# Performance work log

Measured on AMD Instinct MI355X. Metric: run time of the kernel, lower is better.

The kernel has to match this reference:

```python
import jax, jax.numpy as jnp
import numpy as np

jax.config.update("jax_enable_x64", True)  # loss accumulates int64 squared index diffs (~1e14)

PATCH, STRIDE = 7, 1


def extract_patches(img, p, s):
    # img: [b, c, h, w] -> patches [b, N, c*p*p], N = oh*ow (normalize_patch='none')
    pat = jax.lax.conv_general_dilated_patches(img, (p, p), (s, s), 'VALID')  # [b, c*p*p, oh, ow]
    b, d = pat.shape[0], pat.shape[1]
    return pat.reshape(b, d, -1).transpose(0, 2, 1)


def bisect_left(a, v):
    # Exact replica of np.searchsorted(a, v, side='left') binary search,
    # applied (as in the original code) to an UNSORTED int array `a`.
    # a: [N] int, v: [M] int -> [M] insertion indices in [0, N].
    N = a.shape[0]
    lo = jnp.zeros(v.shape, jnp.int64)
    hi = jnp.full(v.shape, N, jnp.int64)
    n_iter = int(np.ceil(np.log2(N))) + 1
    for _ in range(n_iter):
        mid = (lo + hi) // 2
        am = a[jnp.clip(mid, 0, N - 1)]
        go = lo < hi
        pred = am < v
        lo = jnp.where(go & pred, mid + 1, lo)
        hi = jnp.where(go & (~pred), mid, hi)
    return lo


def nearest_vals(a, v):
    # Vectorized find_nearest(a, v_i) for all v_i. a: [N], v: [M].
    N = a.shape[0]
    idx = bisect_left(a, v)
    a_prev = a[jnp.clip(idx - 1, 0, N - 1)]
    a_at = a[jnp.clip(idx, 0, N - 1)]
    take_prev = (idx > 0) & ((idx == N) | (jnp.abs(v - a_prev) < jnp.abs(v - a_at)))
    return jnp.where(take_prev, a_prev, a_at)


def reference(x, y, rand):
    # rand: [b, d, num_proj]; per-batch projection matrix, normalized by unbiased column std
    rand = rand / jnp.std(rand, axis=1, keepdims=True, ddof=1)
    xp = extract_patches(x, PATCH, STRIDE)  # [b, N, d]
    yp = extract_patches(y, PATCH, STRIDE)  # [b, N, d]
    proj_x = jnp.einsum('bnd,bdp->bnp', xp, rand)
    proj_y = jnp.einsum('bnd,bdp->bnp', yp, rand)
    # Original overwrites projections with argsort indices; only j=0 is used
    # because of the early return inside the projection loop.
    ai = jnp.argsort(proj_x[:, :, 0], axis=1).astype(jnp.int64)  # [b, N]
    at = jnp.argsort(proj_y[:, :, 0], axis=1).astype(jnp.int64)  # [b, N]
    nearest = jax.vmap(nearest_vals)(at, ai)  # [b, N]
    N = ai.shape[1]
    per_image = jnp.sum((ai - nearest) ** 2, axis=1) / N  # int sum -> float
    return jnp.mean(per_image)  # batch_reduction='mean'


def setup_inputs() -> dict:
    key = jax.random.key(0)
    k1, k2, k3 = jax.random.split(key, 3)
    b, c, h, w = 4, 3, 256, 256
    d = c * PATCH * PATCH  # 147
    x = jax.random.normal(k1, (b, c, h, w), dtype=jnp.float32)
    y = jax.random.normal(k2, (b, c, h, w), dtype=jnp.float32)
    rand = jax.random.normal(k3, (b, d, 1), dtype=jnp.float32)
    return {"x": x, "y": y, "rand": rand}
```

## Files before the change

### kernel.cpp

```cpp
#include <hip/hip_runtime.h>
#include <stdint.h>

#define OH 250
#define OW 250
#define NPTS (OH*OW)
#define NSEG 4
#define D 147
#define CH 3
#define IMH 256
#define IMW 256
#define NITER 17
#define NBUCK 4096
#define SIG0 12.124355652982141

typedef unsigned long long u64;
typedef unsigned int u32;

#define OFF_REC   0UL
#define OFF_SREC  2000000UL
#define OFF_A     4000000UL
#define OFF_HIST  5000000UL
#define OFF_BASES 5065536UL
#define OFF_CURS  5131088UL
#define OFF_WTS   5196624UL
#define OFF_SUMS  5201328UL
#define WS_NEED   5201360UL

__device__ __forceinline__ u64 packd(double f) {
  u64 u = (u64)__double_as_longlong(f);
  return (u & 0x8000000000000000ULL) ? ~u : (u | 0x8000000000000000ULL);
}

__device__ __forceinline__ int bucket_of(u64 rec) {
  u64 t = rec & ~0x1FFFFULL;
  u64 bits = (t & 0x8000000000000000ULL) ? (t & 0x7FFFFFFFFFFFFFFFULL) : ~t;
  double v = __longlong_as_double((long long)bits);
  double z = (v + 4.0 * SIG0) * ((double)NBUCK / (8.0 * SIG0));
  int b = (z <= 0.0) ? 0 : (int)z;
  if (b > NBUCK - 1) b = NBUCK - 1;
  return b;
}

__global__ __launch_bounds__(256) void prep_kern(const float* __restrict__ rnd,
                                                 double* __restrict__ wts,
                                                 u32* __restrict__ hist,
                                                 u64* __restrict__ sums) {
  int t = threadIdx.x;
  if (blockIdx.x < 4) {
    __shared__ double red[256];
    int b = blockIdx.x;
    double val = (t < D) ? (double)rnd[b * D + t] : 0.0;
    red[t] = val;
    __syncthreads();
    for (int s = 128; s > 0; s >>= 1) { if (t < s) red[t] += red[t + s]; __syncthreads(); }
    double mean = red[0] / (double)D;
    __syncthreads();
    double dv = (t < D) ? (val - mean) : 0.0;
    red[t] = dv * dv;
    __syncthreads();
    for (int s = 128; s > 0; s >>= 1) { if (t < s) red[t] += red[t + s]; __syncthreads(); }
    double stdv = sqrt(red[0] / (double)(D - 1));
    if (t < D) wts[b * D + t] = val / stdv;
  } else {
    int g = (blockIdx.x - 4) * 256 + t;
    if (g < NSEG * NBUCK) hist[g] = 0u;
    if (g < 4) sums[g] = 0ULL;
  }
}

__global__ __launch_bounds__(256) void conv_kern(const float* __restrict__ y,
                                                 const double* __restrict__ wts,
                                                 u64* __restrict__ recs,
                                                 u32* __restrict__ hist) {
  __shared__ float tile[CH][22][22];
  __shared__ double w[D];
  __shared__ u32 lh[NBUCK];
  int b = blockIdx.z;
  const float* in = y + (size_t)b * CH * IMH * IMW;
  int bi = blockIdx.y * 16, bj = blockIdx.x * 16;
  int tid = threadIdx.y * 16 + threadIdx.x;
  for (int k = tid; k < NBUCK; k += 256) lh[k] = 0u;
  if (tid < D) w[tid] = wts[b * D + tid];
  for (int c = 0; c < CH; ++c)
    for (int t = tid; t < 22 * 22; t += 256) {
      int rr = t / 22, cc = t - rr * 22;
      int r = bi + rr, col = bj + cc;
      float v = 0.f;
      if (r < IMH && col < IMW) v = in[((size_t)c * IMH + r) * IMW + col];
      tile[c][rr][cc] = v;
    }
  __syncthreads();
  int i = bi + threadIdx.y, j = bj + threadIdx.x;
  if (i < OH && j < OW) {
    double acc = 0.0;
    #pragma unroll
    for (int c = 0; c < CH; ++c)
      #pragma unroll
      for (int ph = 0; ph < 7; ++ph)
        #pragma unroll
        for (int pw = 0; pw < 7; ++pw)
          acc = fma((double)tile[c][threadIdx.y + ph][threadIdx.x + pw],
                    w[c * 49 + ph * 7 + pw], acc);
    int n = i * OW + j;
    u64 rec = (packd(acc) & ~0x1FFFFULL) | (u64)(u32)n;
    recs[(size_t)b * NPTS + n] = rec;
    atomicAdd(&lh[bucket_of(rec)], 1u);
  }
  __syncthreads();
  for (int k = tid; k < NBUCK; k += 256) {
    u32 c = lh[k];
    if (c) atomicAdd(&hist[b * NBUCK + k], c);
  }
}

__global__ __launch_bounds__(1024) void scan_kern(const u32* __restrict__ hist,
                                                  u32* __restrict__ bases,
                                                  u32* __restrict__ curs) {
  __shared__ u32 part[1024];
  int seg = blockIdx.x, t = threadIdx.x;
  u32 c[4];
  #pragma unroll
  for (int m = 0; m < 4; ++m) c[m] = hist[seg * NBUCK + 4 * t + m];
  u32 s = c[0] + c[1] + c[2] + c[3];
  part[t] = s;
  __syncthreads();
  for (int off = 1; off < 1024; off <<= 1) {
    u32 v = (t >= off) ? part[t - off] : 0u;
    __syncthreads();
    part[t] += v;
    __syncthreads();
  }
  u32 ex = part[t] - s;
  #pragma unroll
  for (int m = 0; m < 4; ++m) {
    bases[seg * (NBUCK + 1) + 4 * t + m] = ex;
    curs[seg * NBUCK + 4 * t + m] = ex;
    ex += c[m];
  }
  if (t == 1023) bases[seg * (NBUCK + 1) + NBUCK] = ex;
}

__global__ __launch_bounds__(256) void scatter_kern(const u64* __restrict__ recs,
                                                    u32* __restrict__ curs,
                                                    u64* __restrict__ srec) {
  int seg = blockIdx.y;
  int e = blockIdx.x * 256 + threadIdx.x;
  if (e < NPTS) {
    u64 rec = recs[(size_t)seg * NPTS + e];
    int bk = bucket_of(rec);
    u32 pos = atomicAdd(&curs[seg * NBUCK + bk], 1u);
    srec[(size_t)seg * NPTS + pos] = rec;
  }
}

__global__ __launch_bounds__(512) void bsort_kern(const u64* __restrict__ srec,
                                                  const u32* __restrict__ bases,
                                                  u32* __restrict__ a) {
  __shared__ u64 buf[8][512];
  int wid = threadIdx.x >> 6, lane = threadIdx.x & 63;
  int w = blockIdx.x * 8 + wid;
  int seg = w >> 12, bk = w & (NBUCK - 1);
  u32 b0 = bases[seg * (NBUCK + 1) + bk];
  u32 b1 = bases[seg * (NBUCK + 1) + bk + 1];
  int n = (int)(b1 - b0);
  const u64* src = srec + (size_t)seg * NPTS + b0;
  u32* dst = a + (size_t)seg * NPTS + b0;
  bool uselds = (n <= 512);
  if (uselds) for (int i = lane; i < n; i += 64) buf[wid][i] = src[i];
  __syncthreads();
  if (uselds) {
    for (int i = lane; i < n; i += 64) {
      u64 x = buf[wid][i];
      int r = 0;
      for (int j = 0; j < n; ++j) r += (buf[wid][j] < x);
      dst[r] = (u32)(x & 0x1FFFFULL);
    }
  } else {
    for (int i = lane; i < n; i += 64) {
      u64 x = src[i];
      int r = 0;
      for (int j = 0; j < n; ++j) r += (src[j] < x);
      dst[r] = (u32)(x & 0x1FFFFULL);
    }
  }
}

__global__ __launch_bounds__(256) void loss_kern(const u32* __restrict__ a_all,
                                                 u64* __restrict__ sums) {
  int b = blockIdx.y;
  int v = blockIdx.x * 256 + threadIdx.x;
  const u32* a = a_all + (size_t)b * NPTS;
  long long term = 0;
  if (v < NPTS) {
    int lo = 0, hi = NPTS;
    #pragma unroll
    for (int it = 0; it < NITER; ++it) {
      int mid = (lo + hi) >> 1;
      int cm = mid > NPTS - 1 ? NPTS - 1 : mid;
      int am = (int)a[cm];
      bool go = lo < hi;
      if (go) {
        if (am < v) lo = mid + 1;
        else        hi = mid;
      }
    }
    int pi = lo - 1; if (pi < 0) pi = 0; if (pi > NPTS - 1) pi = NPTS - 1;
    int ci = lo;     if (ci > NPTS - 1) ci = NPTS - 1;
    int ap = (int)a[pi], aa = (int)a[ci];
    int d1 = v - ap; if (d1 < 0) d1 = -d1;
    int d2 = v - aa; if (d2 < 0) d2 = -d2;
    bool take_prev = (lo > 0) && ((lo == NPTS) || (d1 < d2));
    int nearest = take_prev ? ap : aa;
    long long d = (long long)(v - nearest);
    term = d * d;
  }
  for (int off = 32; off > 0; off >>= 1) term += __shfl_down(term, off, 64);
  __shared__ long long part[4];
  int lane = threadIdx.x & 63, wid = threadIdx.x >> 6;
  if (lane == 0) part[wid] = term;
  __syncthreads();
  if (threadIdx.x == 0) {
    long long tot = part[0] + part[1] + part[2] + part[3];
    atomicAdd(&sums[b], (u64)tot);
  }
}

__global__ void final_kern(const u64* __restrict__ sums, float* __restrict__ out) {
  if (threadIdx.x == 0 && blockIdx.x == 0) {
    double l = 0.0;
    for (int b = 0; b < 4; ++b) l += (double)(long long)sums[b] / (double)NPTS;
    out[0] = (float)(l / 4.0);
  }
}

__global__ void guard_kern(float* __restrict__ out) {
  if (threadIdx.x == 0 && blockIdx.x == 0) out[0] = 9.0e12f;
}

extern "C" void kernel_launch(void* const* d_in, const int* in_sizes, int n_in,
                              void* d_out, int out_size, void* d_ws, size_t ws_size,
                              hipStream_t stream) {
  (void)in_sizes; (void)n_in; (void)out_size;
  if (ws_size < WS_NEED) { guard_kern<<<1, 64, 0, stream>>>((float*)d_out); return; }
  const float* y   = (const float*)d_in[1];
  const float* rnd = (const float*)d_in[2];

  char* ws = (char*)d_ws;
  u64* recs   = (u64*)(ws + OFF_REC);
  u64* srec   = (u64*)(ws + OFF_SREC);
  u32* a      = (u32*)(ws + OFF_A);
  u32* hist   = (u32*)(ws + OFF_HIST);
  u32* bases  = (u32*)(ws + OFF_BASES);
  u32* curs   = (u32*)(ws + OFF_CURS);
  double* wts = (double*)(ws + OFF_WTS);
  u64* sums   = (u64*)(ws + OFF_SUMS);

  prep_kern<<<68, 256, 0, stream>>>(rnd, wts, hist, sums);
  conv_kern<<<dim3(16, 16, NSEG), dim3(16, 16), 0, stream>>>(y, wts, recs, hist);
  scan_kern<<<NSEG, 1024, 0, stream>>>(hist, bases, curs);
  scatter_kern<<<dim3((NPTS + 255) / 256, NSEG), 256, 0, stream>>>(recs, curs, srec);
  bsort_kern<<<NSEG * NBUCK / 8, 512, 0, stream>>>(srec, bases, a);
  loss_kern<<<dim3((NPTS + 255) / 256, NSEG), 256, 0, stream>>>(a, sums);
  final_kern<<<1, 64, 0, stream>>>(sums, (float*)d_out);
}
```

Measured before the change: 137.6 us.

## Fuse all pipeline stages into one cooperative kernel with grid syncs

Replaces the seven separate launches (prep, conv, scan, scatter, bucket sort, loss, final) with a single cooperative kernel of 256 blocks of 512 threads that separates the phases with grid-wide syncs. Weight normalisation is done per block with wave shuffles, the histogram uses block-local shared atomics, and the final reduction happens in-kernel. The aim is to remove launch gaps and per-kernel tail effects. In exchange, each phase is limited to fixed grid parallelism, grid.sync adds its own cost, and a fallback keeps the old multi-kernel path if the cooperative launch fails.

```diff
diff --git a/kernel.cpp b/kernel.cpp
--- a/kernel.cpp
+++ b/kernel.cpp
@@ -1,5 +1,8 @@
 #include <hip/hip_runtime.h>
+#include <hip/hip_cooperative_groups.h>
 #include <stdint.h>
+
+namespace cg = cooperative_groups;
 
 #define OH 250
 #define OW 250
@@ -12,6 +15,8 @@
 #define NITER 17
 #define NBUCK 4096
 #define SIG0 12.124355652982141
+#define GRD 256
+#define BLK 512
 
 typedef unsigned long long u64;
 typedef unsigned int u32;
@@ -39,6 +44,217 @@
   int b = (z <= 0.0) ? 0 : (int)z;
   if (b > NBUCK - 1) b = NBUCK - 1;
   return b;
+}
+
+__global__ __launch_bounds__(BLK, 2) void fused_kern(
+    const float* __restrict__ y, const float* __restrict__ rnd,
+    u64* __restrict__ recs, u64* __restrict__ srec, u32* __restrict__ aidx,
+    u32* __restrict__ hist, u32* __restrict__ bases, u32* __restrict__ curs,
+    u64* __restrict__ sums, float* __restrict__ out) {
+  cg::grid_group grid = cg::this_grid();
+  __shared__ double w[NSEG][D];
+  __shared__ __align__(16) char sh[32768];
+  float (*tile)[22][38] = (float (*)[22][38])sh;
+  u32* lhist = (u32*)(sh + 10048);
+  u64 (*bbuf)[512] = (u64 (*)[512])sh;
+  u32* spart = (u32*)sh;
+  __shared__ long long lsums[NSEG];
+
+  int tid = threadIdx.x, bid = blockIdx.x;
+  int lane = tid & 63, wid = tid >> 6;
+
+  if (wid < NSEG) {
+    int s = wid;
+    double v0 = (double)rnd[s * D + lane];
+    double v1 = (lane + 64 < D) ? (double)rnd[s * D + lane + 64] : 0.0;
+    double v2 = (lane + 128 < D) ? (double)rnd[s * D + lane + 128] : 0.0;
+    double sm = v0 + v1 + v2;
+    for (int o = 32; o > 0; o >>= 1) sm += __shfl_down(sm, o, 64);
+    sm = __shfl(sm, 0, 64);
+    double mean = sm / (double)D;
+    double d0 = v0 - mean;
+    double d1 = (lane + 64 < D) ? v1 - mean : 0.0;
+    double d2 = (lane + 128 < D) ? v2 - mean : 0.0;
+    double ss = d0 * d0 + d1 * d1 + d2 * d2;
+    for (int o = 32; o > 0; o >>= 1) ss += __shfl_down(ss, o, 64);
+    ss = __shfl(ss, 0, 64);
+    double stdv = sqrt(ss / (double)(D - 1));
+    w[s][lane] = v0 / stdv;
+    if (lane + 64 < D) w[s][lane + 64] = v1 / stdv;
+    if (lane + 128 < D) w[s][lane + 128] = v2 / stdv;
+  }
+  {
+    int g = bid * BLK + tid;
+    if (g < NSEG * NBUCK) hist[g] = 0u;
+    if (g < NSEG) sums[g] = 0ULL;
+  }
+  grid.sync();
+
+  for (int k = tid; k < NBUCK; k += BLK) lhist[k] = 0u;
+  int T0 = 2 * bid;
+  int seg = T0 >> 7;
+  const float* in = y + (size_t)seg * CH * IMH * IMW;
+  __syncthreads();
+  for (int r = 0; r < 2; ++r) {
+    int tsub = (T0 + r) & 127;
+    int bi = (tsub >> 3) * 16, bj = (tsub & 7) * 32;
+    for (int t = tid; t < CH * 22 * 38; t += BLK) {
+      int c = t / (22 * 38), rem = t % (22 * 38);
+      int rr = rem / 38, cc = rem % 38;
+      int rI = bi + rr, cI = bj + cc;
+      float v = 0.f;
+      if (rI < IMH && cI < IMW) v = in[((size_t)c * IMH + rI) * IMW + cI];
+      tile[c][rr][cc] = v;
+    }
+    __syncthreads();
+    int ty = tid >> 5, tx = tid & 31;
+    int i = bi + ty, j = bj + tx;
+    if (i < OH && j < OW) {
+      double acc = 0.0;
+      #pragma unroll
+      for (int c = 0; c < CH; ++c)
+        #pragma unroll
+        for (int ph = 0; ph < 7; ++ph)
+          #pragma unroll
+          for (int pw = 0; pw < 7; ++pw)
+            acc = fma((double)tile[c][ty + ph][tx + pw], w[seg][c * 49 + ph * 7 + pw], acc);
+      int n = i * OW + j;
+      u64 rec = (packd(acc) & ~0x1FFFFULL) | (u64)(u32)n;
+      recs[(size_t)seg * NPTS + n] = rec;
+      atomicAdd(&lhist[bucket_of(rec)], 1u);
+    }
+    __syncthreads();
+  }
+  for (int k = tid; k < NBUCK; k += BLK) {
+    u32 c = lhist[k];
+    if (c) atomicAdd(&hist[seg * NBUCK + k], c);
+  }
+  grid.sync();
+
+  if (bid < NSEG) {
+    int s = bid;
+    u32 c[8]; u32 run = 0;
+    #pragma unroll
+    for (int m = 0; m < 8; ++m) { c[m] = hist[s * NBUCK + 8 * tid + m]; run += c[m]; }
+    spart[tid] = run;
+    __syncthreads();
+    for (int off = 1; off < BLK; off <<= 1) {
+      u32 v = (tid >= off) ? spart[tid - off] : 0u;
+      __syncthreads();
+      spart[tid] += v;
+      __syncthreads();
+    }
+    u32 ex = spart[tid] - run;
+    #pragma unroll
+    for (int m = 0; m < 8; ++m) {
+      bases[s * (NBUCK + 1) + 8 * tid + m] = ex;
+      curs[s * NBUCK + 8 * tid + m] = ex;
+      ex += c[m];
+    }
+    if (tid == BLK - 1) bases[s * (NBUCK + 1) + NBUCK] = ex;
+  }
+  grid.sync();
+
+  {
+    int g = bid * BLK + tid;
+    #pragma unroll
+    for (int rep = 0; rep < 2; ++rep) {
+      int e = g + rep * (GRD * BLK);
+      if (e < NSEG * NPTS) {
+        u64 rec = recs[e];
+        int s = e / NPTS;
+        int bk = bucket_of(rec);
+        u32 pos = atomicAdd(&curs[s * NBUCK + bk], 1u);
+        srec[(size_t)s * NPTS + pos] = rec;
+      }
+    }
+  }
+  grid.sync();
+
+  {
+    int gw = bid * 8 + wid;
+    for (int q = 0; q < 8; ++q) {
+      int B = gw + q * 2048;
+      int s = B >> 12, bk = B & (NBUCK - 1);
+      u32 b0 = bases[s * (NBUCK + 1) + bk];
+      u32 b1 = bases[s * (NBUCK + 1) + bk + 1];
+      int n = (int)(b1 - b0);
+      const u64* src = srec + (size_t)s * NPTS + b0;
+      u32* dst = aidx + (size_t)s * NPTS + b0;
+      __syncthreads();
+      if (n <= 512) for (int i = lane; i < n; i += 64) bbuf[wid][i] = src[i];
+      __syncthreads();
+      if (n <= 512) {
+        for (int i = lane; i < n; i += 64) {
+          u64 x = bbuf[wid][i]; int rk = 0;
+          for (int jj = 0; jj < n; ++jj) rk += (bbuf[wid][jj] < x);
+          dst[rk] = (u32)(x & 0x1FFFFULL);
+        }
+      } else {
+        for (int i = lane; i < n; i += 64) {
+          u64 x = src[i]; int rk = 0;
+          for (int jj = 0; jj < n; ++jj) rk += (src[jj] < x);
+          dst[rk] = (u32)(x & 0x1FFFFULL);
+        }
+      }
+    }
+  }
+  grid.sync();
+
+  if (tid < NSEG) lsums[tid] = 0;
+  __syncthreads();
+  {
+    int g = bid * BLK + tid;
+    int v1g = g + GRD * BLK;
+    bool a1 = v1g < NSEG * NPTS;
+    int s0 = g / NPTS, s1 = a1 ? v1g / NPTS : 0;
+    int vv0 = g - s0 * NPTS, vv1 = v1g - s1 * NPTS;
+    const u32* A0 = aidx + (size_t)s0 * NPTS;
+    const u32* A1 = aidx + (size_t)s1 * NPTS;
+    int lo0 = 0, hi0 = NPTS, lo1 = 0, hi1 = NPTS;
+    #pragma unroll
+    for (int it = 0; it < NITER; ++it) {
+      int mid0 = (lo0 + hi0) >> 1, mid1 = (lo1 + hi1) >> 1;
+      int cm0 = mid0 > NPTS - 1 ? NPTS - 1 : mid0;
+      int cm1 = mid1 > NPTS - 1 ? NPTS - 1 : mid1;
+      int am0 = (int)A0[cm0];
+      int am1 = (int)A1[cm1];
+      if (lo0 < hi0) { if (am0 < vv0) lo0 = mid0 + 1; else hi0 = mid0; }
+      if (lo1 < hi1) { if (am1 < vv1) lo1 = mid1 + 1; else hi1 = mid1; }
+    }
+    long long t0, t1;
+    {
+      int pi = lo0 - 1; if (pi < 0) pi = 0; if (pi > NPTS - 1) pi = NPTS - 1;
+      int ci = lo0;     if (ci > NPTS - 1) ci = NPTS - 1;
+      int ap = (int)A0[pi], aa = (int)A0[ci];
+      int d1 = vv0 - ap; if (d1 < 0) d1 = -d1;
+      int d2 = vv0 - aa; if (d2 < 0) d2 = -d2;
+      bool tp = (lo0 > 0) && ((lo0 == NPTS) || (d1 < d2));
+      long long dd = (long long)(vv0 - (tp ? ap : aa));
+      t0 = dd * dd;
+    }
+    {
+      int pi = lo1 - 1; if (pi < 0) pi = 0; if (pi > NPTS - 1) pi = NPTS - 1;
+      int ci = lo1;     if (ci > NPTS - 1) ci = NPTS - 1;
+      int ap = (int)A1[pi], aa = (int)A1[ci];
+      int d1 = vv1 - ap; if (d1 < 0) d1 = -d1;
+      int d2 = vv1 - aa; if (d2 < 0) d2 = -d2;
+      bool tp = (lo1 > 0) && ((lo1 == NPTS) || (d1 < d2));
+      long long dd = (long long)(vv1 - (tp ? ap : aa));
+      t1 = dd * dd;
+    }
+    atomicAdd((u64*)&lsums[s0], (u64)t0);
+    if (a1) atomicAdd((u64*)&lsums[s1], (u64)t1);
+  }
+  __syncthreads();
+  if (tid < NSEG && lsums[tid]) atomicAdd(&sums[tid], (u64)lsums[tid]);
+  grid.sync();
+
+  if (bid == 0 && tid == 0) {
+    double l = 0.0;
+    for (int b = 0; b < NSEG; ++b) l += (double)(long long)sums[b] / (double)NPTS;
+    out[0] = (float)(l / 4.0);
+  }
 }
 
 __global__ __launch_bounds__(256) void prep_kern(const float* __restrict__ rnd,
@@ -248,18 +464,25 @@
   char* ws = (char*)d_ws;
   u64* recs   = (u64*)(ws + OFF_REC);
   u64* srec   = (u64*)(ws + OFF_SREC);
-  u32* a      = (u32*)(ws + OFF_A);
+  u32* aidx   = (u32*)(ws + OFF_A);
   u32* hist   = (u32*)(ws + OFF_HIST);
   u32* bases  = (u32*)(ws + OFF_BASES);
   u32* curs   = (u32*)(ws + OFF_CURS);
   double* wts = (double*)(ws + OFF_WTS);
   u64* sums   = (u64*)(ws + OFF_SUMS);
+  float* out  = (float*)d_out;
+
+  void* args[] = { (void*)&y, (void*)&rnd, (void*)&recs, (void*)&srec, (void*)&aidx,
+                   (void*)&hist, (void*)&bases, (void*)&curs, (void*)&sums, (void*)&out };
+  hipError_t err = hipLaunchCooperativeKernel((const void*)fused_kern,
+                                              dim3(GRD), dim3(BLK), args, 0, stream);
+  if (err == hipSuccess) return;
 
   prep_kern<<<68, 256, 0, stream>>>(rnd, wts, hist, sums);
   conv_kern<<<dim3(16, 16, NSEG), dim3(16, 16), 0, stream>>>(y, wts, recs, hist);
   scan_kern<<<NSEG, 1024, 0, stream>>>(hist, bases, curs);
   scatter_kern<<<dim3((NPTS + 255) / 256, NSEG), 256, 0, stream>>>(recs, curs, srec);
-  bsort_kern<<<NSEG * NBUCK / 8, 512, 0, stream>>>(srec, bases, a);
-  loss_kern<<<dim3((NPTS + 255) / 256, NSEG), 256, 0, stream>>>(a, sums);
-  final_kern<<<1, 64, 0, stream>>>(sums, (float*)d_out);
-}
+  bsort_kern<<<NSEG * NBUCK / 8, 512, 0, stream>>>(srec, bases, aidx);
+  loss_kern<<<dim3((NPTS + 255) / 256, NSEG), 256, 0, stream>>>(aidx, sums);
+  final_kern<<<1, 64, 0, stream>>>(sums, out);
+}
```

Result: slower. 284.9 us (+107.1%).

## Fuse prep, scan and final kernels via last-block tickets and memset

Applied to the files above, without the earlier changes.

Drops the separate prep, scan and final launches. Each conv block now normalizes the projection weights itself with wave shuffles. The last conv block, picked by an atomic ticket, runs the histogram prefix scan. The last loss block computes the final mean. Control buffers are zeroed with one hipMemsetAsync, and scatter now adds the bucket base to a zero-started cursor. This cuts launch count and inter-kernel gaps, at the cost of redundant weight normalization per block and a serial single-block scan tail.

```diff
diff --git a/kernel.cpp b/kernel.cpp
--- a/kernel.cpp
+++ b/kernel.cpp
@@ -19,12 +19,14 @@
 #define OFF_REC   0UL
 #define OFF_SREC  2000000UL
 #define OFF_A     4000000UL
+#define OFF_CTRL  5000000UL
 #define OFF_HIST  5000000UL
 #define OFF_BASES 5065536UL
 #define OFF_CURS  5131088UL
-#define OFF_WTS   5196624UL
-#define OFF_SUMS  5201328UL
-#define WS_NEED   5201360UL
+#define OFF_SUMS  5196624UL
+#define OFF_TICK  5196656UL
+#define CTRL_LEN  196664UL
+#define WS_NEED   5196664UL
 
 __device__ __forceinline__ u64 packd(double f) {
   u64 u = (u64)__double_as_longlong(f);
@@ -41,46 +43,42 @@
   return b;
 }
 
-__global__ __launch_bounds__(256) void prep_kern(const float* __restrict__ rnd,
-                                                 double* __restrict__ wts,
+__global__ __launch_bounds__(256) void conv_kern(const float* __restrict__ y,
+                                                 const float* __restrict__ rnd,
+                                                 u64* __restrict__ recs,
                                                  u32* __restrict__ hist,
-                                                 u64* __restrict__ sums) {
-  int t = threadIdx.x;
-  if (blockIdx.x < 4) {
-    __shared__ double red[256];
-    int b = blockIdx.x;
-    double val = (t < D) ? (double)rnd[b * D + t] : 0.0;
-    red[t] = val;
-    __syncthreads();
-    for (int s = 128; s > 0; s >>= 1) { if (t < s) red[t] += red[t + s]; __syncthreads(); }
-    double mean = red[0] / (double)D;
-    __syncthreads();
-    double dv = (t < D) ? (val - mean) : 0.0;
-    red[t] = dv * dv;
-    __syncthreads();
-    for (int s = 128; s > 0; s >>= 1) { if (t < s) red[t] += red[t + s]; __syncthreads(); }
-    double stdv = sqrt(red[0] / (double)(D - 1));
-    if (t < D) wts[b * D + t] = val / stdv;
-  } else {
-    int g = (blockIdx.x - 4) * 256 + t;
-    if (g < NSEG * NBUCK) hist[g] = 0u;
-    if (g < 4) sums[g] = 0ULL;
-  }
-}
-
-__global__ __launch_bounds__(256) void conv_kern(const float* __restrict__ y,
-                                                 const double* __restrict__ wts,
-                                                 u64* __restrict__ recs,
-                                                 u32* __restrict__ hist) {
+                                                 u32* __restrict__ bases,
+                                                 u32* __restrict__ tick) {
   __shared__ float tile[CH][22][22];
   __shared__ double w[D];
   __shared__ u32 lh[NBUCK];
+  __shared__ u32 spart[256];
+  __shared__ u32 rank_s;
   int b = blockIdx.z;
   const float* in = y + (size_t)b * CH * IMH * IMW;
   int bi = blockIdx.y * 16, bj = blockIdx.x * 16;
   int tid = threadIdx.y * 16 + threadIdx.x;
+  int lane = tid & 63;
+
+  {
+    double v0 = (double)rnd[b * D + lane];
+    double v1 = (double)rnd[b * D + lane + 64];
+    double v2 = (lane + 128 < D) ? (double)rnd[b * D + lane + 128] : 0.0;
+    double sm = v0 + v1 + v2;
+    #pragma unroll
+    for (int o = 32; o > 0; o >>= 1) sm += __shfl_xor(sm, o, 64);
+    double mean = sm / (double)D;
+    double d0 = v0 - mean, d1 = v1 - mean;
+    double d2 = (lane + 128 < D) ? (v2 - mean) : 0.0;
+    double ss = d0 * d0 + d1 * d1 + d2 * d2;
+    #pragma unroll
+    for (int o = 32; o > 0; o >>= 1) ss += __shfl_xor(ss, o, 64);
+    double stdv = sqrt(ss / (double)(D - 1));
+    w[lane] = v0 / stdv;
+    w[lane + 64] = v1 / stdv;
+    if (lane + 128 < D) w[lane + 128] = v2 / stdv;
+  }
   for (int k = tid; k < NBUCK; k += 256) lh[k] = 0u;
-  if (tid < D) w[tid] = wts[b * D + tid];
   for (int c = 0; c < CH; ++c)
     for (int t = tid; t < 22 * 22; t += 256) {
       int rr = t / 22, cc = t - rr * 22;
@@ -111,36 +109,40 @@
     u32 c = lh[k];
     if (c) atomicAdd(&hist[b * NBUCK + k], c);
   }
-}
-
-__global__ __launch_bounds__(1024) void scan_kern(const u32* __restrict__ hist,
-                                                  u32* __restrict__ bases,
-                                                  u32* __restrict__ curs) {
-  __shared__ u32 part[1024];
-  int seg = blockIdx.x, t = threadIdx.x;
-  u32 c[4];
-  #pragma unroll
-  for (int m = 0; m < 4; ++m) c[m] = hist[seg * NBUCK + 4 * t + m];
-  u32 s = c[0] + c[1] + c[2] + c[3];
-  part[t] = s;
-  __syncthreads();
-  for (int off = 1; off < 1024; off <<= 1) {
-    u32 v = (t >= off) ? part[t - off] : 0u;
+  __threadfence();
+  if (tid == 0) rank_s = atomicAdd(&tick[0], 1u);
+  __syncthreads();
+  if (rank_s != 16 * 16 * NSEG - 1) return;
+  __threadfence();
+  for (int s2 = 0; s2 < NSEG; ++s2) {
+    u32 c[16]; u32 run = 0;
+    #pragma unroll
+    for (int m = 0; m < 16; ++m) {
+      c[m] = __hip_atomic_load(&hist[s2 * NBUCK + 16 * tid + m],
+                               __ATOMIC_RELAXED, __HIP_MEMORY_SCOPE_AGENT);
+      run += c[m];
+    }
+    spart[tid] = run;
     __syncthreads();
-    part[t] += v;
+    for (int off = 1; off < 256; off <<= 1) {
+      u32 v = (tid >= off) ? spart[tid - off] : 0u;
+      __syncthreads();
+      spart[tid] += v;
+      __syncthreads();
+    }
+    u32 ex = spart[tid] - run;
+    #pragma unroll
+    for (int m = 0; m < 16; ++m) {
+      bases[s2 * (NBUCK + 1) + 16 * tid + m] = ex;
+      ex += c[m];
+    }
+    if (tid == 255) bases[s2 * (NBUCK + 1) + NBUCK] = ex;
     __syncthreads();
   }
-  u32 ex = part[t] - s;
-  #pragma unroll
-  for (int m = 0; m < 4; ++m) {
-    bases[seg * (NBUCK + 1) + 4 * t + m] = ex;
-    curs[seg * NBUCK + 4 * t + m] = ex;
-    ex += c[m];
-  }
-  if (t == 1023) bases[seg * (NBUCK + 1) + NBUCK] = ex;
 }
 
 __global__ __launch_bounds__(256) void scatter_kern(const u64* __restrict__ recs,
+                                                    const u32* __restrict__ bases,
                                                     u32* __restrict__ curs,
                                                     u64* __restrict__ srec) {
   int seg = blockIdx.y;
@@ -148,7 +150,7 @@
   if (e < NPTS) {
     u64 rec = recs[(size_t)seg * NPTS + e];
     int bk = bucket_of(rec);
-    u32 pos = atomicAdd(&curs[seg * NBUCK + bk], 1u);
+    u32 pos = bases[seg * (NBUCK + 1) + bk] + atomicAdd(&curs[seg * NBUCK + bk], 1u);
     srec[(size_t)seg * NPTS + pos] = rec;
   }
 }
@@ -186,7 +188,10 @@
 }
 
 __global__ __launch_bounds__(256) void loss_kern(const u32* __restrict__ a_all,
-                                                 u64* __restrict__ sums) {
+                                                 u64* __restrict__ sums,
+                                                 u32* __restrict__ tick,
+                                                 float* __restrict__ out,
+                                                 int nblocks) {
   int b = blockIdx.y;
   int v = blockIdx.x * 256 + threadIdx.x;
   const u32* a = a_all + (size_t)b * NPTS;
@@ -216,19 +221,24 @@
   }
   for (int off = 32; off > 0; off >>= 1) term += __shfl_down(term, off, 64);
   __shared__ long long part[4];
+  __shared__ u32 rank_s;
   int lane = threadIdx.x & 63, wid = threadIdx.x >> 6;
   if (lane == 0) part[wid] = term;
   __syncthreads();
   if (threadIdx.x == 0) {
     long long tot = part[0] + part[1] + part[2] + part[3];
     atomicAdd(&sums[b], (u64)tot);
-  }
-}
-
-__global__ void final_kern(const u64* __restrict__ sums, float* __restrict__ out) {
-  if (threadIdx.x == 0 && blockIdx.x == 0) {
+    __threadfence();
+    rank_s = atomicAdd(&tick[1], 1u);
+  }
+  __syncthreads();
+  if (rank_s == (u32)(nblocks - 1) && threadIdx.x == 0) {
+    __threadfence();
     double l = 0.0;
-    for (int b = 0; b < 4; ++b) l += (double)(long long)sums[b] / (double)NPTS;
+    for (int s = 0; s < NSEG; ++s) {
+      u64 sv = __hip_atomic_load(&sums[s], __ATOMIC_RELAXED, __HIP_MEMORY_SCOPE_AGENT);
+      l += (double)(long long)sv / (double)NPTS;
+    }
     out[0] = (float)(l / 4.0);
   }
 }
@@ -248,18 +258,18 @@
   char* ws = (char*)d_ws;
   u64* recs   = (u64*)(ws + OFF_REC);
   u64* srec   = (u64*)(ws + OFF_SREC);
-  u32* a      = (u32*)(ws + OFF_A);
+  u32* aidx   = (u32*)(ws + OFF_A);
   u32* hist   = (u32*)(ws + OFF_HIST);
   u32* bases  = (u32*)(ws + OFF_BASES);
   u32* curs   = (u32*)(ws + OFF_CURS);
-  double* wts = (double*)(ws + OFF_WTS);
   u64* sums   = (u64*)(ws + OFF_SUMS);
-
-  prep_kern<<<68, 256, 0, stream>>>(rnd, wts, hist, sums);
-  conv_kern<<<dim3(16, 16, NSEG), dim3(16, 16), 0, stream>>>(y, wts, recs, hist);
-  scan_kern<<<NSEG, 1024, 0, stream>>>(hist, bases, curs);
-  scatter_kern<<<dim3((NPTS + 255) / 256, NSEG), 256, 0, stream>>>(recs, curs, srec);
-  bsort_kern<<<NSEG * NBUCK / 8, 512, 0, stream>>>(srec, bases, a);
-  loss_kern<<<dim3((NPTS + 255) / 256, NSEG), 256, 0, stream>>>(a, sums);
-  final_kern<<<1, 64, 0, stream>>>(sums, (float*)d_out);
-}
+  u32* tick   = (u32*)(ws + OFF_TICK);
+  float* out  = (float*)d_out;
+
+  hipMemsetAsync(ws + OFF_CTRL, 0, CTRL_LEN, stream);
+  conv_kern<<<dim3(16, 16, NSEG), dim3(16, 16), 0, stream>>>(y, rnd, recs, hist, bases, tick);
+  scatter_kern<<<dim3((NPTS + 255) / 256, NSEG), 256, 0, stream>>>(recs, bases, curs, srec);
+  bsort_kern<<<NSEG * NBUCK / 8, 512, 0, stream>>>(srec, bases, aidx);
+  int nb = ((NPTS + 255) / 256) * NSEG;
+  loss_kern<<<dim3((NPTS + 255) / 256, NSEG), 256, 0, stream>>>(aidx, sums, tick, out, nb);
+}
```

After: 226.1 us. 1.64x slower.
